# Performance work log

Measured on AMD Instinct MI355X. Metric: run time of the kernel, lower is better.

Reference implementation:

```python
import jax, jax.numpy as jnp
import numpy as np
import math

D_MODEL = 1024
N_HEAD = 16
D_HEAD = D_MODEL // N_HEAD
INIT_SIZE = 1200  # RelativeSinusoidalPositionalEmbedding init_size
SCALE = 1.0       # scale=False in __init__


def _rel_pos_embed(L, d_head):
    """Replicates RelativeSinusoidalPositionalEmbedding: table over positions
    [-601, 600] (num=init_size+1=1201 rows), padding row 0 zeroed, then gather
    rows for positions arange(-L/2, L/2) + origin_shift (origin_shift=601)."""
    num = INIT_SIZE + 1                      # 1201
    half = d_head // 2
    freq = jnp.exp(jnp.arange(half, dtype=jnp.float32) * (-math.log(10000.0) / (half - 1)))
    pos_vals = jnp.arange(-num // 2, num // 2, dtype=jnp.float32)   # -601..599 -> 1201 vals
    ang = pos_vals[:, None] * freq[None, :]
    table = jnp.concatenate([jnp.sin(ang), jnp.cos(ang)], axis=1)   # [num, d_head]
    table = table.at[0].set(0.0)             # padding_idx = 0
    origin_shift = num // 2 + 1              # 601
    idx = jnp.arange(-(L // 2), L // 2) + origin_shift   # L even -> L indices
    return table[idx]                        # [L, d_head]


def setup_inputs() -> dict:
    key = jax.random.key(0)
    k1, k2, k3, k4, k5 = jax.random.split(key, 5)
    B, L = 4, 1024
    embed = jax.random.normal(k1, (B, L, D_MODEL), dtype=jnp.float32)
    umask = jnp.ones((B, L), dtype=jnp.int32)                       # 1 = valid utterance
    qmask = jax.random.randint(k2, (B, L), 0, 2).astype(jnp.int64)  # speaker ids {0,1}
    W_qkv = jax.random.normal(k3, (D_MODEL, 4 * D_MODEL), dtype=jnp.float32) * 0.02
    W_pos = jax.random.normal(k4, (D_HEAD, 3 * D_MODEL), dtype=jnp.float32) * 0.02
    W_fc  = jax.random.normal(k5, (D_MODEL, D_MODEL), dtype=jnp.float32) * 0.02
    return {"embed": embed, "umask": umask, "qmask": qmask,
            "W_qkv": W_qkv, "W_pos": W_pos, "W_fc": W_fc}


def reference(embed, umask, qmask, W_qkv, W_pos, W_fc):
    B, L, d = embed.shape
    H, dh = N_HEAD, d // N_HEAD

    # qkv projection and head split
    q, k1, k2, v = jnp.split(embed @ W_qkv, 4, axis=-1)             # each [B, L, d]
    q  = q.reshape(B, L, H, dh).transpose(0, 2, 1, 3)               # [B, H, L, dh]
    k1 = k1.reshape(B, L, H, dh).transpose(0, 2, 1, 3)
    k2 = k2.reshape(B, L, H, dh).transpose(0, 2, 1, 3)
    v  = v.reshape(B, L, H, dh).transpose(0, 2, 1, 3)

    # relative position projections (detached sinusoids -> qk_pos linear)
    pe = _rel_pos_embed(L, dh)                                      # [L, dh]
    qp, kp1, kp2 = jnp.split(pe @ W_pos, 3, axis=-1)                # each [L, d]
    qp  = qp.reshape(L, H, dh).transpose(1, 0, 2)                   # [H, L, dh]
    kp1 = kp1.reshape(L, H, dh).transpose(1, 0, 2)
    kp2 = kp2.reshape(L, H, dh).transpose(1, 0, 2)

    pos1 = jnp.einsum('hqd,hkd->hqk', qp, kp1)                      # [H, L, L]
    pos2 = jnp.einsum('hqd,hkd->hqk', qp, kp2)

    attn_self  = jnp.einsum('bhqd,bhkd->bhqk', q, k1) + pos1[None]  # [B, H, L, L]
    attn_other = jnp.einsum('bhqd,bhkd->bhqk', q, k2) + pos2[None]

    # same-speaker mask: self-attn only where speakers match, other-attn where they differ
    qeq = (qmask[:, :, None] == qmask[:, None, :])                  # [B, L, L] bool
    attn_self  = jnp.where(qeq[:, None], attn_self, 0.0)
    attn_other = jnp.where(qeq[:, None], 0.0, attn_other)
    attn_add = (attn_self + attn_other) / SCALE

    # causal (order) mask + padding mask (eval-mode path of the module)
    order = jnp.triu(jnp.ones((L, L), dtype=bool), 1)[None] | (umask == 0)[:, None, :]
    attn = jnp.where(order[:, None], -jnp.inf, attn_add)
    p = jax.nn.softmax(attn, axis=-1)                               # dropout is identity in eval

    out = jnp.einsum('bhqk,bhkd->bhqd', p, v)                       # [B, H, L, dh]
    out = out.transpose(0, 2, 1, 3).reshape(B, L, d)
    return out @ W_fc
```

## Files before the change

kernel.cpp:

```cpp
#include <hip/hip_runtime.h>
#include <math.h>

#define NB 4
#define SEQ 1024
#define DMODEL 1024
#define NHEAD 16
#define DHEAD 64

typedef __attribute__((ext_vector_type(8))) short s16x8;
typedef __attribute__((ext_vector_type(4))) short s16x4;
typedef __attribute__((ext_vector_type(4))) float f32x4;

__device__ __forceinline__ short f2bf(float f) {
    union { float f; unsigned u; } x; x.f = f;
    unsigned r = x.u + 0x7fffu + ((x.u >> 16) & 1u);
    return (short)(r >> 16);
}

__device__ __forceinline__ unsigned cvtpk(float lo, float hi) {
    unsigned r;
    asm("v_cvt_pk_bf16_f32 %0, %1, %2" : "=v"(r) : "v"(lo), "v"(hi));
    return r;
}

__device__ __forceinline__ f32x4 mfma16(s16x8 a, s16x8 b, f32x4 c) {
    return __builtin_amdgcn_mfma_f32_16x16x32_bf16(a, b, c, 0, 0, 0);
}

__device__ __forceinline__ s16x8 cvt8(float4 a, float4 b) {
    s16x8 v;
    v[0] = f2bf(a.x); v[1] = f2bf(a.y); v[2] = f2bf(a.z); v[3] = f2bf(a.w);
    v[4] = f2bf(b.x); v[5] = f2bf(b.y); v[6] = f2bf(b.z); v[7] = f2bf(b.w);
    return v;
}

__device__ __forceinline__ s16x8 ldlds(const short* base, int byteoff) {
    return *(const s16x8*)((const char*)base + byteoff);
}

#define GLDS16(g, l) __builtin_amdgcn_global_load_lds( \
    (const __attribute__((address_space(1))) unsigned int*)(g), \
    (__attribute__((address_space(3))) unsigned int*)(l), 16, 0, 0)
#define GLDS4(g, l) __builtin_amdgcn_global_load_lds( \
    (const __attribute__((address_space(1))) unsigned int*)(g), \
    (__attribute__((address_space(3))) unsigned int*)(l), 4, 0, 0)

__global__ __launch_bounds__(256) void prep_a_kernel(
    const float* __restrict__ embed, const float* __restrict__ Wqkv,
    short* __restrict__ ebf, short* __restrict__ WqkvT)
{
    __shared__ __align__(16) char smem[9216];
    int gb = blockIdx.x;
    int tid = threadIdx.x;

    if (gb < 2048) {
        int i = (gb * 256 + tid) * 8;
        float4 a = *(const float4*)(embed + i);
        float4 b = *(const float4*)(embed + i + 4);
        *(s16x8*)(ebf + i) = cvt8(a, b);
    } else {
        int t = gb - 2048;
        int bx = t & 63, by = t >> 6;
        const int N = 4096;
        short (*T)[72] = (short(*)[72])smem;
        int nt = bx * 64, kt = by * 64;
        int kl = tid >> 4;
        int nl = (tid & 15) * 4;
        #pragma unroll
        for (int rr = 0; rr < 4; ++rr) {
            int k = kl + rr * 16;
            float4 v = *(const float4*)(Wqkv + (size_t)(kt + k) * N + nt + nl);
            T[nl + 0][k] = f2bf(v.x);
            T[nl + 1][k] = f2bf(v.y);
            T[nl + 2][k] = f2bf(v.z);
            T[nl + 3][k] = f2bf(v.w);
        }
        __syncthreads();
        int nr = tid >> 2;
        int kc = (tid & 3) * 16;
        uint4 a = *(const uint4*)&T[nr][kc];
        uint4 b = *(const uint4*)&T[nr][kc + 8];
        short* dst = WqkvT + (size_t)(nt + nr) * 1024 + kt + kc;
        *(uint4*)(dst) = a;
        *(uint4*)(dst + 8) = b;
    }
}

__global__ __launch_bounds__(256) void gemm_qkv_fused(
    const short* __restrict__ A, const short* __restrict__ BT,
    short* __restrict__ o0, short* __restrict__ o1, short* __restrict__ o2,
    short* __restrict__ o3,
    const int* __restrict__ qmask, const int* __restrict__ umask,
    const float* __restrict__ Wpos, const float* __restrict__ Wfc,
    int* __restrict__ PM, short* __restrict__ qpb, short* __restrict__ WfcT)
{
    __shared__ short As[2][128 * 32];
    __shared__ short Bs[2][128 * 32];

    int gb = blockIdx.x;
    int tid = threadIdx.x;

    if (gb < 644) {
        char* smem = (char*)&As[0][0];
        if (gb < 4) {
            int b = gb;
            for (int k = tid; k < 1088; k += 256) {
                int v = 2;
                if (k < 1024)
                    v = (qmask[b * 1024 + k] & 1) | ((umask[b * 1024 + k] == 0) ? 2 : 0);
                PM[b * 1088 + k] = v;
            }
        } else if (gb < 388) {
            int bid = gb - 4;
            int s = bid >> 7;
            int l0 = (bid & 127) * 8;
            float (*pe)[64] = (float(*)[64])smem;

            for (int idx = tid; idx < 512; idx += 256) {
                int li = idx >> 6, t = idx & 63;
                float p = (float)(l0 + li - 512);
                int j = (t < 32) ? t : (t - 32);
                float f = expf(-0.2971077539f * (float)j);
                float a = p * f;
                pe[li][t] = (t < 32) ? sinf(a) : cosf(a);
            }
            __syncthreads();

            float acc[4][8] = {};
            const float* wp = Wpos + s * 1024 + tid;
            for (int t = 0; t < 64; ++t) {
                float w0 = wp[t * 3072];
                float w1 = wp[t * 3072 + 256];
                float w2 = wp[t * 3072 + 512];
                float w3 = wp[t * 3072 + 768];
                #pragma unroll
                for (int li = 0; li < 8; ++li) {
                    float pv = pe[li][t];
                    acc[0][li] += pv * w0; acc[1][li] += pv * w1;
                    acc[2][li] += pv * w2; acc[3][li] += pv * w3;
                }
            }
            #pragma unroll
            for (int cc = 0; cc < 4; ++cc) {
                int c = tid + cc * 256;
                int h = c >> 6, d = c & 63;
                #pragma unroll
                for (int li = 0; li < 8; ++li) {
                    short bv = f2bf(acc[cc][li]);
                    if (s == 0) {
                        qpb[((size_t)(h << 10) + l0 + li) * 64 + d] = bv;
                    } else {
                        short* dst = (s == 1) ? o1 : o2;
                        #pragma unroll
                        for (int bb = 0; bb < 4; ++bb)
                            dst[((size_t)((bb * 16 + h) * 1024) + l0 + li) * 128 + 64 + d] = bv;
                    }
                }
            }
        } else {
            int t = gb - 388;
            int bx = t & 15, by = t >> 4;
            const int N = 1024;
            short (*T)[72] = (short(*)[72])smem;
            int nt = bx * 64, kt = by * 64;
            int kl = tid >> 4;
            int nl = (tid & 15) * 4;
            #pragma unroll
            for (int rr = 0; rr < 4; ++rr) {
                int k = kl + rr * 16;
                float4 v = *(const float4*)(Wfc + (size_t)(kt + k) * N + nt + nl);
                T[nl + 0][k] = f2bf(v.x);
                T[nl + 1][k] = f2bf(v.y);
                T[nl + 2][k] = f2bf(v.z);
                T[nl + 3][k] = f2bf(v.w);
            }
            __syncthreads();
            int nr = tid >> 2;
            int kc = (tid & 3) * 16;
            uint4 a = *(const uint4*)&T[nr][kc];
            uint4 b = *(const uint4*)&T[nr][kc + 8];
            short* dst = WfcT + (size_t)(nt + nr) * 1024 + kt + kc;
            *(uint4*)(dst) = a;
            *(uint4*)(dst + 8) = b;
        }
        return;
    }

    int lin = gb - 644;
    int cpx = 1024 >> 3;
    int swb = (lin & 7) * cpx + (lin >> 3);
    int bx = swb & 31, by = swb >> 5;
    int m0 = by * 128, n0 = bx * 128;

    int w = tid >> 6, lane = tid & 63;
    int wm = w >> 1, wn = w & 1;
    int lq = lane & 15, lg = lane >> 4;

    f32x4 zero = {0.f, 0.f, 0.f, 0.f};
    f32x4 acc[4][4];
    #pragma unroll
    for (int i = 0; i < 4; ++i)
        #pragma unroll
        for (int j = 0; j < 4; ++j) acc[i][j] = zero;

    int swz = (((lane & 3) ^ ((lane >> 2) & 3)) << 3);
    int srow = lane >> 2;
    const short* aBase = A  + (size_t)(m0 + (w << 5) + srow) * 1024 + swz;
    const short* bBase = BT + (size_t)(n0 + (w << 5) + srow) * 1024 + swz;
    int dOff = w * 1024;

    GLDS16(aBase, &As[0][dOff]);
    GLDS16(aBase + 16 * 1024, &As[0][dOff + 512]);
    GLDS16(bBase, &Bs[0][dOff]);
    GLDS16(bBase + 16 * 1024, &Bs[0][dOff + 512]);

    int cur = 0;
    for (int kt = 0; kt < 1024; kt += 32) {
        if (kt + 32 < 1024) {
            int nxt = cur ^ 1;
            GLDS16(aBase + kt + 32, &As[nxt][dOff]);
            GLDS16(aBase + kt + 32 + 16 * 1024, &As[nxt][dOff + 512]);
            GLDS16(bBase + kt + 32, &Bs[nxt][dOff]);
            GLDS16(bBase + kt + 32 + 16 * 1024, &Bs[nxt][dOff + 512]);
            asm volatile("s_waitcnt vmcnt(4)" ::: "memory");
        } else {
            asm volatile("s_waitcnt vmcnt(0)" ::: "memory");
        }
        __builtin_amdgcn_s_barrier();
        asm volatile("" ::: "memory");

        s16x8 af[4], bfr[4];
        #pragma unroll
        for (int mt = 0; mt < 4; ++mt) {
            int row = wm * 64 + mt * 16 + lq;
            af[mt] = ldlds(As[cur], (row * 64 + lg * 16) ^ ((row & 3) << 4));
        }
        #pragma unroll
        for (int nt = 0; nt < 4; ++nt) {
            int row = wn * 64 + nt * 16 + lq;
            bfr[nt] = ldlds(Bs[cur], (row * 64 + lg * 16) ^ ((row & 3) << 4));
        }
        #pragma unroll
        for (int mt = 0; mt < 4; ++mt)
            #pragma unroll
            for (int nt = 0; nt < 4; ++nt)
                acc[mt][nt] = mfma16(af[mt], bfr[nt], acc[mt][nt]);

        asm volatile("" ::: "memory");
        __builtin_amdgcn_s_barrier();
        cur ^= 1;
    }

    #pragma unroll
    for (int nt = 0; nt < 4; ++nt) {
        int n = n0 + wn * 64 + nt * 16 + lq;
        int sec = n >> 10, hd = n & 1023;
        int hh = hd >> 6, d = hd & 63;
        #pragma unroll
        for (int mt = 0; mt < 4; ++mt) {
            int mb = m0 + wm * 64 + mt * 16 + lg * 4;
            int b = mb >> 10, li0 = mb & 1023;
            int bh = b * 16 + hh;
            if (sec == 3) {
                s16x4 pv;
                #pragma unroll
                for (int r = 0; r < 4; ++r) pv[r] = f2bf(acc[mt][nt][r]);
                *(s16x4*)(o3 + (((size_t)(bh * 64 + d)) << 10) + li0) = pv;
            } else {
                #pragma unroll
                for (int r = 0; r < 4; ++r) {
                    short bv = f2bf(acc[mt][nt][r]);
                    if (sec == 0)
                        o0[((size_t)(bh << 10) + li0 + r) * 64 + d] = bv;
                    else if (sec == 1)
                        o1[((size_t)bh * 1024 + li0 + r) * 128 + d] = bv;
                    else
                        o2[((size_t)bh * 1024 + li0 + r) * 128 + d] = bv;
                }
            }
        }
    }
}

template<int EPI, int NCOLS>
__global__ __launch_bounds__(256) void gemm_nt(
    const short* __restrict__ A, const short* __restrict__ BT,
    float* __restrict__ of)
{
    __shared__ short As[2][128 * 32];
    __shared__ short Bs[2][128 * 32];

    int nwg = gridDim.x * gridDim.y;
    int lin = blockIdx.y * gridDim.x + blockIdx.x;
    int cpx = nwg >> 3;
    int swb = (lin & 7) * cpx + (lin >> 3);
    int bx = swb % gridDim.x, by = swb / gridDim.x;
    int m0 = by * 128, n0 = bx * 128;

    int tid = threadIdx.x;
    int w = tid >> 6, lane = tid & 63;
    int wm = w >> 1, wn = w & 1;
    int lq = lane & 15, lg = lane >> 4;

    f32x4 zero = {0.f, 0.f, 0.f, 0.f};
    f32x4 acc[4][4];
    #pragma unroll
    for (int i = 0; i < 4; ++i)
        #pragma unroll
        for (int j = 0; j < 4; ++j) acc[i][j] = zero;

    int swz = (((lane & 3) ^ ((lane >> 2) & 3)) << 3);
    int srow = lane >> 2;
    const short* aBase = A  + (size_t)(m0 + (w << 5) + srow) * 1024 + swz;
    const short* bBase = BT + (size_t)(n0 + (w << 5) + srow) * 1024 + swz;
    int dOff = w * 1024;

    GLDS16(aBase, &As[0][dOff]);
    GLDS16(aBase + 16 * 1024, &As[0][dOff + 512]);
    GLDS16(bBase, &Bs[0][dOff]);
    GLDS16(bBase + 16 * 1024, &Bs[0][dOff + 512]);

    int cur = 0;
    for (int kt = 0; kt < 1024; kt += 32) {
        if (kt + 32 < 1024) {
            int nxt = cur ^ 1;
            GLDS16(aBase + kt + 32, &As[nxt][dOff]);
            GLDS16(aBase + kt + 32 + 16 * 1024, &As[nxt][dOff + 512]);
            GLDS16(bBase + kt + 32, &Bs[nxt][dOff]);
            GLDS16(bBase + kt + 32 + 16 * 1024, &Bs[nxt][dOff + 512]);
            asm volatile("s_waitcnt vmcnt(4)" ::: "memory");
        } else {
            asm volatile("s_waitcnt vmcnt(0)" ::: "memory");
        }
        __builtin_amdgcn_s_barrier();
        asm volatile("" ::: "memory");

        s16x8 af[4], bfr[4];
        #pragma unroll
        for (int mt = 0; mt < 4; ++mt) {
            int row = wm * 64 + mt * 16 + lq;
            af[mt] = ldlds(As[cur], (row * 64 + lg * 16) ^ ((row & 3) << 4));
        }
        #pragma unroll
        for (int nt = 0; nt < 4; ++nt) {
            int row = wn * 64 + nt * 16 + lq;
            bfr[nt] = ldlds(Bs[cur], (row * 64 + lg * 16) ^ ((row & 3) << 4));
        }
        #pragma unroll
        for (int mt = 0; mt < 4; ++mt)
            #pragma unroll
            for (int nt = 0; nt < 4; ++nt)
                acc[mt][nt] = mfma16(af[mt], bfr[nt], acc[mt][nt]);

        asm volatile("" ::: "memory");
        __builtin_amdgcn_s_barrier();
        cur ^= 1;
    }

    #pragma unroll
    for (int nt = 0; nt < 4; ++nt) {
        int n = n0 + wn * 64 + nt * 16 + lq;
        #pragma unroll
        for (int mt = 0; mt < 4; ++mt) {
            int mb = m0 + wm * 64 + mt * 16 + lg * 4;
            #pragma unroll
            for (int r = 0; r < 4; ++r)
                of[(size_t)(mb + r) * NCOLS + n] = acc[mt][nt][r];
        }
    }
}

__global__ __launch_bounds__(256) void attn_kernel(
    const short* __restrict__ qb, const short* __restrict__ k1cat,
    const short* __restrict__ k2cat, const short* __restrict__ vtb,
    const short* __restrict__ qpb, const int* __restrict__ PM,
    const int* __restrict__ qmask, short* __restrict__ ctx)
{
    __shared__ short K1s[2][32 * 128];
    __shared__ short K2s[2][32 * 128];
    __shared__ short Vs[2][64 * 32];
    __shared__ int   PMs[2][64];

    int bid = blockIdx.x;
    int xg = bid & 7, j = bid >> 3;
    int bh = xg * 8 + (j & 7);
    int qt = 15 - (j >> 3);
    int b = bh >> 4, h = bh & 15;

    int w = threadIdx.x >> 6, lane = threadIdx.x & 63;
    int lq = lane & 15, lg = lane >> 4;

    auto STAGE = [&](int d, int K0) {
        #pragma unroll
        for (int i = 0; i < 5; ++i) {
            int g = w * 5 + i;
            if (g < 8) {
                int row = g * 4 + (lane >> 4);
                int colb = ((lane & 15) << 4) ^ ((row & 7) << 4);
                const short* src = k1cat + ((size_t)bh * 1024 + K0 + row) * 128 + (colb >> 1);
                GLDS16(src, &K1s[d][g * 512]);
            } else if (g < 16) {
                int gg = g - 8;
                int row = gg * 4 + (lane >> 4);
                int colb = ((lane & 15) << 4) ^ ((row & 7) << 4);
                const short* src = k2cat + ((size_t)bh * 1024 + K0 + row) * 128 + (colb >> 1);
                GLDS16(src, &K2s[d][gg * 512]);
            } else {
                int c = g - 16;
                int row = c * 16 + (lane >> 2);
                int colb = ((lane & 3) << 4) ^ ((row & 3) << 4);
                const short* src = vtb + ((size_t)bh * 64 + row) * 1024 + K0 + (colb >> 1);
                GLDS16(src, &Vs[d][c * 512]);
            }
        }
        if (w == 0) {
            GLDS4(PM + b * 1088 + K0 + lane, &PMs[d][0]);
        }
    };

    f32x4 zero = {0.f, 0.f, 0.f, 0.f};

    int q0 = qt * 64 + w * 16;
    int q_glob = q0 + lq;

    const short* qrow  = qb  + ((size_t)bh * SEQ + q_glob) * DHEAD;
    const short* qprow = qpb + ((size_t)h  * SEQ + q_glob) * DHEAD;
    s16x8 qf0  = *(const s16x8*)(qrow + lg * 8);
    s16x8 qf1  = *(const s16x8*)(qrow + 32 + lg * 8);
    s16x8 qpf0 = *(const s16x8*)(qprow + lg * 8);
    s16x8 qpf1 = *(const s16x8*)(qprow + 32 + lg * 8);
    int qm_q = qmask[b * SEQ + q_glob] & 1;
    asm volatile("s_waitcnt vmcnt(0)" ::: "memory");

    f32x4 accO[4];
    #pragma unroll
    for (int i = 0; i < 4; ++i) accO[i] = zero;
    float m_run = -1e30f, l_run = 0.f;

    int nslab = 2 * qt + 2;
    STAGE(0, 0);

    #pragma unroll 1
    for (int t = 0; t < nslab; ++t) {
        int cur = t & 1;
        if (t + 1 < nslab) {
            STAGE(cur ^ 1, (t + 1) * 32);
            if (w == 0) asm volatile("s_waitcnt vmcnt(6)" ::: "memory");
            else        asm volatile("s_waitcnt vmcnt(5)" ::: "memory");
        } else {
            asm volatile("s_waitcnt vmcnt(0)" ::: "memory");
        }
        __builtin_amdgcn_s_barrier();
        asm volatile("" ::: "memory");

        int K0 = t * 32;
        if (K0 <= q0 + 15) {
            const short* b1 = K1s[cur];
            const short* b2 = K2s[cur];

            f32x4 s1v[2], s2v[2];
            __builtin_amdgcn_s_setprio(1);
            #pragma unroll
            for (int hh = 0; hh < 2; ++hh) {
                int row = hh * 16 + lq;
                int ro = row * 256 + (lg << 4);
                int sw = (row & 7) << 4;
                f32x4 tv = zero, uv = zero;
                tv = mfma16(ldlds(b1, (ro      ) ^ sw), qf0,  tv);
                tv = mfma16(ldlds(b1, (ro +  64) ^ sw), qf1,  tv);
                tv = mfma16(ldlds(b1, (ro + 128) ^ sw), qpf0, tv);
                tv = mfma16(ldlds(b1, (ro + 192) ^ sw), qpf1, tv);
                s1v[hh] = tv;
                uv = mfma16(ldlds(b2, (ro      ) ^ sw), qf0,  uv);
                uv = mfma16(ldlds(b2, (ro +  64) ^ sw), qf1,  uv);
                uv = mfma16(ldlds(b2, (ro + 128) ^ sw), qpf0, uv);
                uv = mfma16(ldlds(b2, (ro + 192) ^ sw), qpf1, uv);
                s2v[hh] = uv;
            }
            __builtin_amdgcn_s_setprio(0);

            int4 pmv0 = *(const int4*)&PMs[cur][lg * 4];
            int4 pmv1 = *(const int4*)&PMs[cur][16 + lg * 4];
            int pme[8] = {pmv0.x, pmv0.y, pmv0.z, pmv0.w,
                          pmv1.x, pmv1.y, pmv1.z, pmv1.w};

            float sv[8];
            #pragma unroll
            for (int i = 0; i < 8; ++i) {
                int hh = i >> 2, r = i & 3;
                int k_idx = K0 + hh * 16 + lg * 4 + r;
                int pm = pme[i];
                float s = ((pm & 1) == qm_q) ? s1v[hh][r] : s2v[hh][r];
                if (k_idx > q_glob || (pm & 2)) s = -INFINITY;
                sv[i] = s;
            }
            float tm = sv[0];
            #pragma unroll
            for (int i = 1; i < 8; ++i) tm = fmaxf(tm, sv[i]);
            tm = fmaxf(tm, __shfl_xor(tm, 16));
            tm = fmaxf(tm, __shfl_xor(tm, 32));

            if (!__all(tm <= m_run + 8.0f)) {
                float m_new = fmaxf(m_run, tm);
                float scale = __expf(m_run - m_new);
                m_run = m_new;
                l_run *= scale;
                f32x4 scv;
                scv[0] = __shfl(scale, lg * 4 + 0);
                scv[1] = __shfl(scale, lg * 4 + 1);
                scv[2] = __shfl(scale, lg * 4 + 2);
                scv[3] = __shfl(scale, lg * 4 + 3);
                #pragma unroll
                for (int dt = 0; dt < 4; ++dt) accO[dt] *= scv;
            }

            float p[8]; float ps = 0.f;
            #pragma unroll
            for (int i = 0; i < 8; ++i) { p[i] = __expf(sv[i] - m_run); ps += p[i]; }
            ps += __shfl_xor(ps, 16);
            ps += __shfl_xor(ps, 32);
            l_run += ps;

            unsigned dA0 = cvtpk(p[0], p[1]);
            unsigned dA1 = cvtpk(p[2], p[3]);
            unsigned dB0 = cvtpk(p[4], p[5]);
            unsigned dB1 = cvtpk(p[6], p[7]);
            int sl0 = lq + ((lg & 1) << 5);
            int sl1 = sl0 + 16;
            unsigned a0 = (unsigned)__shfl((int)dA0, sl0), a1 = (unsigned)__shfl((int)dA1, sl0);
            unsigned a2 = (unsigned)__shfl((int)dA0, sl1), a3 = (unsigned)__shfl((int)dA1, sl1);
            unsigned c0 = (unsigned)__shfl((int)dB0, sl0), c1 = (unsigned)__shfl((int)dB1, sl0);
            unsigned c2 = (unsigned)__shfl((int)dB0, sl1), c3 = (unsigned)__shfl((int)dB1, sl1);
            bool hi = (lg >= 2);
            union { unsigned u[4]; s16x8 v; } pa;
            pa.u[0] = hi ? c0 : a0; pa.u[1] = hi ? c1 : a1;
            pa.u[2] = hi ? c2 : a2; pa.u[3] = hi ? c3 : a3;

            __builtin_amdgcn_s_setprio(1);
            #pragma unroll
            for (int dt = 0; dt < 4; ++dt) {
                int vrow = dt * 16 + lq;
                int voff = (vrow * 64 + (lg << 4)) ^ ((vrow & 3) << 4);
                accO[dt] = mfma16(pa.v, ldlds(Vs[cur], voff), accO[dt]);
            }
            __builtin_amdgcn_s_setprio(0);
        }

        asm volatile("" ::: "memory");
        __builtin_amdgcn_s_barrier();
    }

    float inv = 1.0f / l_run;
    f32x4 invv;
    invv[0] = __shfl(inv, lg * 4 + 0);
    invv[1] = __shfl(inv, lg * 4 + 1);
    invv[2] = __shfl(inv, lg * 4 + 2);
    invv[3] = __shfl(inv, lg * 4 + 3);
    #pragma unroll
    for (int dt = 0; dt < 4; ++dt) {
        #pragma unroll
        for (int r = 0; r < 4; ++r) {
            int qo = q0 + lg * 4 + r;
            size_t off = ((size_t)(b * SEQ + qo)) * DMODEL + h * DHEAD + dt * 16 + lq;
            ctx[off] = f2bf(accO[dt][r] * invv[r]);
        }
    }
}

extern "C" void kernel_launch(void* const* d_in, const int* in_sizes, int n_in,
                              void* d_out, int out_size, void* d_ws, size_t ws_size,
                              hipStream_t stream) {
    const float* embed = (const float*)d_in[0];
    const int*   umask = (const int*)d_in[1];
    const int*   qmask = (const int*)d_in[2];
    const float* Wqkv  = (const float*)d_in[3];
    const float* Wpos  = (const float*)d_in[4];
    const float* Wfc   = (const float*)d_in[5];
    float* out = (float*)d_out;

    char* w = (char*)d_ws;
    short* qb    = (short*)(w + (0ull  << 20));
    short* vtb   = (short*)(w + (8ull  << 20));
    short* qpb   = (short*)(w + (16ull << 20));
    short* ctx   = (short*)(w + (18ull << 20));
    short* ebf   = ctx;
    short* k1cat = (short*)(w + (26ull << 20));
    short* k2cat = (short*)(w + (42ull << 20));
    int*   PM    = (int*)  (w + (58ull << 20));
    short* WqkvT = (short*)(w + (59ull << 20));
    short* WfcT  = (short*)(w + (67ull << 20));

    hipLaunchKernelGGL(prep_a_kernel, dim3(3072), dim3(256), 0, stream,
                       embed, Wqkv, ebf, WqkvT);
    hipLaunchKernelGGL(gemm_qkv_fused, dim3(1668), dim3(256), 0, stream,
                       ebf, WqkvT, qb, k1cat, k2cat, vtb,
                       qmask, umask, Wpos, Wfc, PM, qpb, WfcT);
    hipLaunchKernelGGL(attn_kernel, dim3(1024), dim3(256), 0, stream,
                       qb, k1cat, k2cat, vtb, qpb, PM, qmask, ctx);
    hipLaunchKernelGGL((gemm_nt<1, 1024>), dim3(8, 32), dim3(256), 0, stream,
                       ctx, WfcT, out);
}
```

Measured before the change: 162.3 us.

## Process two query tiles per attention block and reorder fused GEMM block roles

The attention kernel now has each wave handle two 16-row query groups, 64 rows apart, so every staged K1/K2/V slab in LDS is reused by twice as many queries, and the grid is halved to 512 blocks. This cuts global-to-LDS staging traffic and barriers per query, at the cost of more registers (two accumulator sets), possible lower occupancy, and coarser causal work balance. Separately, the fused QKV GEMM kernel now gives the GEMM tiles the low block indices and the auxiliary prep work (mask, positional projection, Wfc transpose) the high indices, so GEMM tiles are dispatched first.

```diff
diff --git a/kernel.cpp b/kernel.cpp
--- a/kernel.cpp
+++ b/kernel.cpp
@@ -100,18 +100,19 @@
     int gb = blockIdx.x;
     int tid = threadIdx.x;
 
-    if (gb < 644) {
+    if (gb >= 1024) {
+        int pb = gb - 1024;
         char* smem = (char*)&As[0][0];
-        if (gb < 4) {
-            int b = gb;
+        if (pb < 4) {
+            int b = pb;
             for (int k = tid; k < 1088; k += 256) {
                 int v = 2;
                 if (k < 1024)
                     v = (qmask[b * 1024 + k] & 1) | ((umask[b * 1024 + k] == 0) ? 2 : 0);
                 PM[b * 1088 + k] = v;
             }
-        } else if (gb < 388) {
-            int bid = gb - 4;
+        } else if (pb < 388) {
+            int bid = pb - 4;
             int s = bid >> 7;
             int l0 = (bid & 127) * 8;
             float (*pe)[64] = (float(*)[64])smem;
@@ -158,7 +159,7 @@
                 }
             }
         } else {
-            int t = gb - 388;
+            int t = pb - 388;
             int bx = t & 15, by = t >> 4;
             const int N = 1024;
             short (*T)[72] = (short(*)[72])smem;
@@ -186,7 +187,7 @@
         return;
     }
 
-    int lin = gb - 644;
+    int lin = gb;
     int cpx = 1024 >> 3;
     int swb = (lin & 7) * cpx + (lin >> 3);
     int bx = swb & 31, by = swb >> 5;
@@ -370,6 +371,108 @@
     }
 }
 
+#define QKM(S1, S2, QF0, QF1, QPF0, QPF1) {                                   \
+    _Pragma("unroll")                                                         \
+    for (int hh = 0; hh < 2; ++hh) {                                          \
+        int row = hh * 16 + lq;                                               \
+        int ro = row * 256 + (lg << 4);                                       \
+        int sw = (row & 7) << 4;                                              \
+        f32x4 tv = zero, uv = zero;                                           \
+        tv = mfma16(ldlds(b1, (ro      ) ^ sw), QF0,  tv);                    \
+        tv = mfma16(ldlds(b1, (ro +  64) ^ sw), QF1,  tv);                    \
+        tv = mfma16(ldlds(b1, (ro + 128) ^ sw), QPF0, tv);                    \
+        tv = mfma16(ldlds(b1, (ro + 192) ^ sw), QPF1, tv);                    \
+        S1[hh] = tv;                                                          \
+        uv = mfma16(ldlds(b2, (ro      ) ^ sw), QF0,  uv);                    \
+        uv = mfma16(ldlds(b2, (ro +  64) ^ sw), QF1,  uv);                    \
+        uv = mfma16(ldlds(b2, (ro + 128) ^ sw), QPF0, uv);                    \
+        uv = mfma16(ldlds(b2, (ro + 192) ^ sw), QPF1, uv);                    \
+        S2[hh] = uv;                                                          \
+    }                                                                         \
+}
+
+#define FIN(S1, S2, QMQ, QGLOB, ACCO, MRUN, LRUN) {                           \
+    int pme[8] = {pmv0.x, pmv0.y, pmv0.z, pmv0.w,                             \
+                  pmv1.x, pmv1.y, pmv1.z, pmv1.w};                            \
+    float sv[8];                                                              \
+    _Pragma("unroll")                                                         \
+    for (int i = 0; i < 8; ++i) {                                             \
+        int hh = i >> 2, r = i & 3;                                           \
+        int k_idx = K0 + hh * 16 + lg * 4 + r;                                \
+        int pm = pme[i];                                                      \
+        float s = ((pm & 1) == (QMQ)) ? S1[hh][r] : S2[hh][r];                \
+        if (k_idx > (QGLOB) || (pm & 2)) s = -INFINITY;                       \
+        sv[i] = s;                                                            \
+    }                                                                         \
+    float tm = sv[0];                                                         \
+    _Pragma("unroll")                                                         \
+    for (int i = 1; i < 8; ++i) tm = fmaxf(tm, sv[i]);                        \
+    tm = fmaxf(tm, __shfl_xor(tm, 16));                                       \
+    tm = fmaxf(tm, __shfl_xor(tm, 32));                                       \
+    if (!__all(tm <= MRUN + 8.0f)) {                                          \
+        float mn = fmaxf(MRUN, tm);                                           \
+        float sc = __expf(MRUN - mn);                                         \
+        MRUN = mn; LRUN *= sc;                                                \
+        f32x4 scv;                                                            \
+        scv[0] = __shfl(sc, lg * 4 + 0);                                      \
+        scv[1] = __shfl(sc, lg * 4 + 1);                                      \
+        scv[2] = __shfl(sc, lg * 4 + 2);                                      \
+        scv[3] = __shfl(sc, lg * 4 + 3);                                      \
+        _Pragma("unroll")                                                     \
+        for (int dt = 0; dt < 4; ++dt) ACCO[dt] *= scv;                       \
+    }                                                                         \
+    float p[8]; float ps = 0.f;                                               \
+    _Pragma("unroll")                                                         \
+    for (int i = 0; i < 8; ++i) { p[i] = __expf(sv[i] - MRUN); ps += p[i]; }  \
+    ps += __shfl_xor(ps, 16);                                                 \
+    ps += __shfl_xor(ps, 32);                                                 \
+    LRUN += ps;                                                               \
+    unsigned dA0 = cvtpk(p[0], p[1]);                                         \
+    unsigned dA1 = cvtpk(p[2], p[3]);                                         \
+    unsigned dB0 = cvtpk(p[4], p[5]);                                         \
+    unsigned dB1 = cvtpk(p[6], p[7]);                                         \
+    int sl0 = lq + ((lg & 1) << 5);                                           \
+    int sl1 = sl0 + 16;                                                       \
+    unsigned a0 = (unsigned)__shfl((int)dA0, sl0);                            \
+    unsigned a1 = (unsigned)__shfl((int)dA1, sl0);                            \
+    unsigned a2 = (unsigned)__shfl((int)dA0, sl1);                            \
+    unsigned a3 = (unsigned)__shfl((int)dA1, sl1);                            \
+    unsigned c0 = (unsigned)__shfl((int)dB0, sl0);                            \
+    unsigned c1 = (unsigned)__shfl((int)dB1, sl0);                            \
+    unsigned c2 = (unsigned)__shfl((int)dB0, sl1);                            \
+    unsigned c3 = (unsigned)__shfl((int)dB1, sl1);                            \
+    bool hi = (lg >= 2);                                                      \
+    union { unsigned u[4]; s16x8 v; } pa;                                     \
+    pa.u[0] = hi ? c0 : a0; pa.u[1] = hi ? c1 : a1;                           \
+    pa.u[2] = hi ? c2 : a2; pa.u[3] = hi ? c3 : a3;                           \
+    __builtin_amdgcn_s_setprio(1);                                            \
+    _Pragma("unroll")                                                         \
+    for (int dt = 0; dt < 4; ++dt) {                                          \
+        int vrow = dt * 16 + lq;                                              \
+        int voff = (vrow * 64 + (lg << 4)) ^ ((vrow & 3) << 4);               \
+        ACCO[dt] = mfma16(pa.v, ldlds(Vs[cur], voff), ACCO[dt]);              \
+    }                                                                         \
+    __builtin_amdgcn_s_setprio(0);                                            \
+}
+
+#define EPIW(ACCO, LRUN, Q0) {                                                \
+    float inv = 1.0f / (LRUN);                                                \
+    f32x4 invv;                                                               \
+    invv[0] = __shfl(inv, lg * 4 + 0);                                        \
+    invv[1] = __shfl(inv, lg * 4 + 1);                                        \
+    invv[2] = __shfl(inv, lg * 4 + 2);                                        \
+    invv[3] = __shfl(inv, lg * 4 + 3);                                        \
+    _Pragma("unroll")                                                         \
+    for (int dt = 0; dt < 4; ++dt) {                                          \
+        _Pragma("unroll")                                                     \
+        for (int r = 0; r < 4; ++r) {                                         \
+            int qo = (Q0) + lg * 4 + r;                                       \
+            size_t off = ((size_t)(b * SEQ + qo)) * DMODEL + h * DHEAD + dt * 16 + lq; \
+            ctx[off] = f2bf(ACCO[dt][r] * invv[r]);                           \
+        }                                                                     \
+    }                                                                         \
+}
+
 __global__ __launch_bounds__(256) void attn_kernel(
     const short* __restrict__ qb, const short* __restrict__ k1cat,
     const short* __restrict__ k2cat, const short* __restrict__ vtb,
@@ -384,7 +487,7 @@
     int bid = blockIdx.x;
     int xg = bid & 7, j = bid >> 3;
     int bh = xg * 8 + (j & 7);
-    int qt = 15 - (j >> 3);
+    int qt = 7 - (j >> 3);
     int b = bh >> 4, h = bh & 15;
 
     int w = threadIdx.x >> 6, lane = threadIdx.x & 63;
@@ -420,24 +523,32 @@
 
     f32x4 zero = {0.f, 0.f, 0.f, 0.f};
 
-    int q0 = qt * 64 + w * 16;
-    int q_glob = q0 + lq;
-
-    const short* qrow  = qb  + ((size_t)bh * SEQ + q_glob) * DHEAD;
-    const short* qprow = qpb + ((size_t)h  * SEQ + q_glob) * DHEAD;
-    s16x8 qf0  = *(const s16x8*)(qrow + lg * 8);
-    s16x8 qf1  = *(const s16x8*)(qrow + 32 + lg * 8);
-    s16x8 qpf0 = *(const s16x8*)(qprow + lg * 8);
-    s16x8 qpf1 = *(const s16x8*)(qprow + 32 + lg * 8);
-    int qm_q = qmask[b * SEQ + q_glob] & 1;
+    int q0A = qt * 128 + w * 16;
+    int q0B = q0A + 64;
+    int qgA = q0A + lq, qgB = q0B + lq;
+
+    const short* qrowA  = qb  + ((size_t)bh * SEQ + qgA) * DHEAD;
+    const short* qprowA = qpb + ((size_t)h  * SEQ + qgA) * DHEAD;
+    const short* qrowB  = qb  + ((size_t)bh * SEQ + qgB) * DHEAD;
+    const short* qprowB = qpb + ((size_t)h  * SEQ + qgB) * DHEAD;
+    s16x8 qf0A  = *(const s16x8*)(qrowA + lg * 8);
+    s16x8 qf1A  = *(const s16x8*)(qrowA + 32 + lg * 8);
+    s16x8 qpf0A = *(const s16x8*)(qprowA + lg * 8);
+    s16x8 qpf1A = *(const s16x8*)(qprowA + 32 + lg * 8);
+    s16x8 qf0B  = *(const s16x8*)(qrowB + lg * 8);
+    s16x8 qf1B  = *(const s16x8*)(qrowB + 32 + lg * 8);
+    s16x8 qpf0B = *(const s16x8*)(qprowB + lg * 8);
+    s16x8 qpf1B = *(const s16x8*)(qprowB + 32 + lg * 8);
+    int qmA = qmask[b * SEQ + qgA] & 1;
+    int qmB = qmask[b * SEQ + qgB] & 1;
     asm volatile("s_waitcnt vmcnt(0)" ::: "memory");
 
-    f32x4 accO[4];
+    f32x4 accA[4], accB[4];
     #pragma unroll
-    for (int i = 0; i < 4; ++i) accO[i] = zero;
-    float m_run = -1e30f, l_run = 0.f;
-
-    int nslab = 2 * qt + 2;
+    for (int i = 0; i < 4; ++i) { accA[i] = zero; accB[i] = zero; }
+    float mA = -1e30f, lA = 0.f, mB = -1e30f, lB = 0.f;
+
+    int nslab = 4 * qt + 4;
     STAGE(0, 0);
 
     #pragma unroll 1
@@ -454,117 +565,29 @@
         asm volatile("" ::: "memory");
 
         int K0 = t * 32;
-        if (K0 <= q0 + 15) {
-            const short* b1 = K1s[cur];
-            const short* b2 = K2s[cur];
-
-            f32x4 s1v[2], s2v[2];
-            __builtin_amdgcn_s_setprio(1);
-            #pragma unroll
-            for (int hh = 0; hh < 2; ++hh) {
-                int row = hh * 16 + lq;
-                int ro = row * 256 + (lg << 4);
-                int sw = (row & 7) << 4;
-                f32x4 tv = zero, uv = zero;
-                tv = mfma16(ldlds(b1, (ro      ) ^ sw), qf0,  tv);
-                tv = mfma16(ldlds(b1, (ro +  64) ^ sw), qf1,  tv);
-                tv = mfma16(ldlds(b1, (ro + 128) ^ sw), qpf0, tv);
-                tv = mfma16(ldlds(b1, (ro + 192) ^ sw), qpf1, tv);
-                s1v[hh] = tv;
-                uv = mfma16(ldlds(b2, (ro      ) ^ sw), qf0,  uv);
-                uv = mfma16(ldlds(b2, (ro +  64) ^ sw), qf1,  uv);
-                uv = mfma16(ldlds(b2, (ro + 128) ^ sw), qpf0, uv);
-                uv = mfma16(ldlds(b2, (ro + 192) ^ sw), qpf1, uv);
-                s2v[hh] = uv;
-            }
-            __builtin_amdgcn_s_setprio(0);
-
-            int4 pmv0 = *(const int4*)&PMs[cur][lg * 4];
-            int4 pmv1 = *(const int4*)&PMs[cur][16 + lg * 4];
-            int pme[8] = {pmv0.x, pmv0.y, pmv0.z, pmv0.w,
-                          pmv1.x, pmv1.y, pmv1.z, pmv1.w};
-
-            float sv[8];
-            #pragma unroll
-            for (int i = 0; i < 8; ++i) {
-                int hh = i >> 2, r = i & 3;
-                int k_idx = K0 + hh * 16 + lg * 4 + r;
-                int pm = pme[i];
-                float s = ((pm & 1) == qm_q) ? s1v[hh][r] : s2v[hh][r];
-                if (k_idx > q_glob || (pm & 2)) s = -INFINITY;
-                sv[i] = s;
-            }
-            float tm = sv[0];
-            #pragma unroll
-            for (int i = 1; i < 8; ++i) tm = fmaxf(tm, sv[i]);
-            tm = fmaxf(tm, __shfl_xor(tm, 16));
-            tm = fmaxf(tm, __shfl_xor(tm, 32));
-
-            if (!__all(tm <= m_run + 8.0f)) {
-                float m_new = fmaxf(m_run, tm);
-                float scale = __expf(m_run - m_new);
-                m_run = m_new;
-                l_run *= scale;
-                f32x4 scv;
-                scv[0] = __shfl(scale, lg * 4 + 0);
-                scv[1] = __shfl(scale, lg * 4 + 1);
-                scv[2] = __shfl(scale, lg * 4 + 2);
-                scv[3] = __shfl(scale, lg * 4 + 3);
-                #pragma unroll
-                for (int dt = 0; dt < 4; ++dt) accO[dt] *= scv;
-            }
-
-            float p[8]; float ps = 0.f;
-            #pragma unroll
-            for (int i = 0; i < 8; ++i) { p[i] = __expf(sv[i] - m_run); ps += p[i]; }
-            ps += __shfl_xor(ps, 16);
-            ps += __shfl_xor(ps, 32);
-            l_run += ps;
-
-            unsigned dA0 = cvtpk(p[0], p[1]);
-            unsigned dA1 = cvtpk(p[2], p[3]);
-            unsigned dB0 = cvtpk(p[4], p[5]);
-            unsigned dB1 = cvtpk(p[6], p[7]);
-            int sl0 = lq + ((lg & 1) << 5);
-            int sl1 = sl0 + 16;
-            unsigned a0 = (unsigned)__shfl((int)dA0, sl0), a1 = (unsigned)__shfl((int)dA1, sl0);
-            unsigned a2 = (unsigned)__shfl((int)dA0, sl1), a3 = (unsigned)__shfl((int)dA1, sl1);
-            unsigned c0 = (unsigned)__shfl((int)dB0, sl0), c1 = (unsigned)__shfl((int)dB1, sl0);
-            unsigned c2 = (unsigned)__shfl((int)dB0, sl1), c3 = (unsigned)__shfl((int)dB1, sl1);
-            bool hi = (lg >= 2);
-            union { unsigned u[4]; s16x8 v; } pa;
-            pa.u[0] = hi ? c0 : a0; pa.u[1] = hi ? c1 : a1;
-            pa.u[2] = hi ? c2 : a2; pa.u[3] = hi ? c3 : a3;
-
-            __builtin_amdgcn_s_setprio(1);
-            #pragma unroll
-            for (int dt = 0; dt < 4; ++dt) {
-                int vrow = dt * 16 + lq;
-                int voff = (vrow * 64 + (lg << 4)) ^ ((vrow & 3) << 4);
-                accO[dt] = mfma16(pa.v, ldlds(Vs[cur], voff), accO[dt]);
-            }
-            __builtin_amdgcn_s_setprio(0);
-        }
+        bool doA = (K0 <= q0A + 15);
+        bool doB = (K0 <= q0B + 15);
+        const short* b1 = K1s[cur];
+        const short* b2 = K2s[cur];
+
+        int4 pmv0 = *(const int4*)&PMs[cur][lg * 4];
+        int4 pmv1 = *(const int4*)&PMs[cur][16 + lg * 4];
+
+        f32x4 s1A[2], s2A[2], s1B[2], s2B[2];
+        __builtin_amdgcn_s_setprio(1);
+        if (doA) QKM(s1A, s2A, qf0A, qf1A, qpf0A, qpf1A);
+        if (doB) QKM(s1B, s2B, qf0B, qf1B, qpf0B, qpf1B);
+        __builtin_amdgcn_s_setprio(0);
+
+        if (doA) FIN(s1A, s2A, qmA, qgA, accA, mA, lA);
+        if (doB) FIN(s1B, s2B, qmB, qgB, accB, mB, lB);
 
         asm volatile("" ::: "memory");
         __builtin_amdgcn_s_barrier();
     }
 
-    float inv = 1.0f / l_run;
-    f32x4 invv;
-    invv[0] = __shfl(inv, lg * 4 + 0);
-    invv[1] = __shfl(inv, lg * 4 + 1);
-    invv[2] = __shfl(inv, lg * 4 + 2);
-    invv[3] = __shfl(inv, lg * 4 + 3);
-    #pragma unroll
-    for (int dt = 0; dt < 4; ++dt) {
-        #pragma unroll
-        for (int r = 0; r < 4; ++r) {
-            int qo = q0 + lg * 4 + r;
-            size_t off = ((size_t)(b * SEQ + qo)) * DMODEL + h * DHEAD + dt * 16 + lq;
-            ctx[off] = f2bf(accO[dt][r] * invv[r]);
-        }
-    }
+    EPIW(accA, lA, q0A);
+    EPIW(accB, lB, q0B);
 }
 
 extern "C" void kernel_launch(void* const* d_in, const int* in_sizes, int n_in,
@@ -595,7 +618,7 @@
     hipLaunchKernelGGL(gemm_qkv_fused, dim3(1668), dim3(256), 0, stream,
                        ebf, WqkvT, qb, k1cat, k2cat, vtb,
                        qmask, umask, Wpos, Wfc, PM, qpb, WfcT);
-    hipLaunchKernelGGL(attn_kernel, dim3(1024), dim3(256), 0, stream,
+    hipLaunchKernelGGL(attn_kernel, dim3(512), dim3(256), 0, stream,
                        qb, k1cat, k2cat, vtb, qpb, PM, qmask, ctx);
     hipLaunchKernelGGL((gemm_nt<1, 1024>), dim3(8, 32), dim3(256), 0, stream,
                        ctx, WfcT, out);
```

Result: slower. 198.7 us (+22.4%).

## Load V and mask directly to registers in attention; reorder GEMM block dispatch

Applied to the files above, without the earlier changes.

In the attention kernel, V fragments and the padding/speaker mask are now loaded straight from global memory into registers each slab instead of being staged through LDS via global_load_lds. This shrinks shared memory and staging instructions and removes LDS reads, and the kernel gets a min-waves-per-EU hint of 4. The wait count is adjusted to the new number of in-flight async loads. Separately, the fused QKV GEMM kernel now puts the GEMM tiles on the low block indices and the prep work (mask, positional projection, Wfc transpose) at the end, so GEMM blocks are dispatched first. Loads issued every slab, including slabs skipped by the causal check, add global traffic and latency exposure, and the per-thread V loads are no longer double-buffered.

```diff
diff --git a/kernel.cpp b/kernel.cpp
--- a/kernel.cpp
+++ b/kernel.cpp
@@ -41,9 +41,6 @@
 #define GLDS16(g, l) __builtin_amdgcn_global_load_lds( \
     (const __attribute__((address_space(1))) unsigned int*)(g), \
     (__attribute__((address_space(3))) unsigned int*)(l), 16, 0, 0)
-#define GLDS4(g, l) __builtin_amdgcn_global_load_lds( \
-    (const __attribute__((address_space(1))) unsigned int*)(g), \
-    (__attribute__((address_space(3))) unsigned int*)(l), 4, 0, 0)
 
 __global__ __launch_bounds__(256) void prep_a_kernel(
     const float* __restrict__ embed, const float* __restrict__ Wqkv,
@@ -100,18 +97,19 @@
     int gb = blockIdx.x;
     int tid = threadIdx.x;
 
-    if (gb < 644) {
+    if (gb >= 1024) {
+        int pb = gb - 1024;
         char* smem = (char*)&As[0][0];
-        if (gb < 4) {
-            int b = gb;
+        if (pb < 4) {
+            int b = pb;
             for (int k = tid; k < 1088; k += 256) {
                 int v = 2;
                 if (k < 1024)
                     v = (qmask[b * 1024 + k] & 1) | ((umask[b * 1024 + k] == 0) ? 2 : 0);
                 PM[b * 1088 + k] = v;
             }
-        } else if (gb < 388) {
-            int bid = gb - 4;
+        } else if (pb < 388) {
+            int bid = pb - 4;
             int s = bid >> 7;
             int l0 = (bid & 127) * 8;
             float (*pe)[64] = (float(*)[64])smem;
@@ -158,7 +156,7 @@
                 }
             }
         } else {
-            int t = gb - 388;
+            int t = pb - 388;
             int bx = t & 15, by = t >> 4;
             const int N = 1024;
             short (*T)[72] = (short(*)[72])smem;
@@ -186,7 +184,7 @@
         return;
     }
 
-    int lin = gb - 644;
+    int lin = gb;
     int cpx = 1024 >> 3;
     int swb = (lin & 7) * cpx + (lin >> 3);
     int bx = swb & 31, by = swb >> 5;
@@ -370,7 +368,7 @@
     }
 }
 
-__global__ __launch_bounds__(256) void attn_kernel(
+__global__ __launch_bounds__(256, 4) void attn_kernel(
     const short* __restrict__ qb, const short* __restrict__ k1cat,
     const short* __restrict__ k2cat, const short* __restrict__ vtb,
     const short* __restrict__ qpb, const int* __restrict__ PM,
@@ -378,8 +376,6 @@
 {
     __shared__ short K1s[2][32 * 128];
     __shared__ short K2s[2][32 * 128];
-    __shared__ short Vs[2][64 * 32];
-    __shared__ int   PMs[2][64];
 
     int bid = blockIdx.x;
     int xg = bid & 7, j = bid >> 3;
@@ -392,29 +388,21 @@
 
     auto STAGE = [&](int d, int K0) {
         #pragma unroll
-        for (int i = 0; i < 5; ++i) {
-            int g = w * 5 + i;
+        for (int i = 0; i < 4; ++i) {
+            int g = w * 4 + i;
+            int row, colb;
             if (g < 8) {
-                int row = g * 4 + (lane >> 4);
-                int colb = ((lane & 15) << 4) ^ ((row & 7) << 4);
+                row = g * 4 + (lane >> 4);
+                colb = ((lane & 15) << 4) ^ ((row & 7) << 4);
                 const short* src = k1cat + ((size_t)bh * 1024 + K0 + row) * 128 + (colb >> 1);
                 GLDS16(src, &K1s[d][g * 512]);
-            } else if (g < 16) {
+            } else {
                 int gg = g - 8;
-                int row = gg * 4 + (lane >> 4);
-                int colb = ((lane & 15) << 4) ^ ((row & 7) << 4);
+                row = gg * 4 + (lane >> 4);
+                colb = ((lane & 15) << 4) ^ ((row & 7) << 4);
                 const short* src = k2cat + ((size_t)bh * 1024 + K0 + row) * 128 + (colb >> 1);
                 GLDS16(src, &K2s[d][gg * 512]);
-            } else {
-                int c = g - 16;
-                int row = c * 16 + (lane >> 2);
-                int colb = ((lane & 3) << 4) ^ ((row & 3) << 4);
-                const short* src = vtb + ((size_t)bh * 64 + row) * 1024 + K0 + (colb >> 1);
-                GLDS16(src, &Vs[d][c * 512]);
-            }
-        }
-        if (w == 0) {
-            GLDS4(PM + b * 1088 + K0 + lane, &PMs[d][0]);
+            }
         }
     };
 
@@ -430,6 +418,10 @@
     s16x8 qpf0 = *(const s16x8*)(qprow + lg * 8);
     s16x8 qpf1 = *(const s16x8*)(qprow + 32 + lg * 8);
     int qm_q = qmask[b * SEQ + q_glob] & 1;
+
+    const short* vbase = vtb + (size_t)bh * 64 * 1024;
+    const int*   pmb   = PM + b * 1088;
+
     asm volatile("s_waitcnt vmcnt(0)" ::: "memory");
 
     f32x4 accO[4];
@@ -443,17 +435,24 @@
     #pragma unroll 1
     for (int t = 0; t < nslab; ++t) {
         int cur = t & 1;
+        int K0 = t * 32;
+
+        s16x8 vf[4];
+        #pragma unroll
+        for (int dt = 0; dt < 4; ++dt)
+            vf[dt] = *(const s16x8*)(vbase + (size_t)(dt * 16 + lq) * 1024 + K0 + lg * 8);
+        int4 pmv0 = *(const int4*)(pmb + K0 + lg * 4);
+        int4 pmv1 = *(const int4*)(pmb + K0 + 16 + lg * 4);
+
         if (t + 1 < nslab) {
             STAGE(cur ^ 1, (t + 1) * 32);
-            if (w == 0) asm volatile("s_waitcnt vmcnt(6)" ::: "memory");
-            else        asm volatile("s_waitcnt vmcnt(5)" ::: "memory");
+            asm volatile("s_waitcnt vmcnt(4)" ::: "memory");
         } else {
             asm volatile("s_waitcnt vmcnt(0)" ::: "memory");
         }
         __builtin_amdgcn_s_barrier();
         asm volatile("" ::: "memory");
 
-        int K0 = t * 32;
         if (K0 <= q0 + 15) {
             const short* b1 = K1s[cur];
             const short* b2 = K2s[cur];
@@ -479,8 +478,6 @@
             }
             __builtin_amdgcn_s_setprio(0);
 
-            int4 pmv0 = *(const int4*)&PMs[cur][lg * 4];
-            int4 pmv1 = *(const int4*)&PMs[cur][16 + lg * 4];
             int pme[8] = {pmv0.x, pmv0.y, pmv0.z, pmv0.w,
                           pmv1.x, pmv1.y, pmv1.z, pmv1.w};
 
@@ -538,11 +535,8 @@
 
             __builtin_amdgcn_s_setprio(1);
             #pragma unroll
-            for (int dt = 0; dt < 4; ++dt) {
-                int vrow = dt * 16 + lq;
-                int voff = (vrow * 64 + (lg << 4)) ^ ((vrow & 3) << 4);
-                accO[dt] = mfma16(pa.v, ldlds(Vs[cur], voff), accO[dt]);
-            }
+            for (int dt = 0; dt < 4; ++dt)
+                accO[dt] = mfma16(pa.v, vf[dt], accO[dt]);
             __builtin_amdgcn_s_setprio(0);
         }
 
```

Measured after the change: 172.1 us. +6.1%, slower.
